# Optimization experiments

Hardware: AMD Instinct MI355X
Metric: run time of the kernel (lower is better)

Reference implementation:

```python
import jax, jax.numpy as jnp
import numpy as np

N, C, W_DIM, H_DIM = 2, 256, 64, 64
HEADS = 4
DH = C // HEADS  # per-head dim for Q,K,V projections
EPS = 1e-5


def _layernorm(x, w, b):
    mu = jnp.mean(x, axis=-1, keepdims=True)
    var = jnp.var(x, axis=-1, keepdims=True)
    return (x - mu) * jax.lax.rsqrt(var + EPS) * w + b


def setup_inputs() -> dict:
    key = jax.random.key(0)
    ks = jax.random.split(key, 12)
    s = 1.0 / np.sqrt(C)
    return {
        "x": jax.random.normal(ks[0], (N, C, W_DIM, H_DIM), dtype=jnp.float32),
        "ln1_w": jnp.ones((C,), jnp.float32),
        "ln1_b": jnp.zeros((C,), jnp.float32),
        # per-head projection weights, laid out for x @ W: [heads, C, DH]
        "WQ": jax.random.normal(ks[1], (HEADS, C, DH), jnp.float32) * s,
        "WK": jax.random.normal(ks[2], (HEADS, C, DH), jnp.float32) * s,
        "WV": jax.random.normal(ks[3], (HEADS, C, DH), jnp.float32) * s,
        "ln2_w": jnp.ones((C,), jnp.float32),
        "ln2_b": jnp.zeros((C,), jnp.float32),
        "W1": jax.random.normal(ks[4], (C, C), jnp.float32) * s,
        "b1": jnp.zeros((C,), jnp.float32),
        "W2": jax.random.normal(ks[5], (C, C), jnp.float32) * s,
        "b2": jnp.zeros((C,), jnp.float32),
    }


def reference(x, ln1_w, ln1_b, WQ, WK, WV, ln2_w, ln2_b, W1, b1, W2, b2):
    n, c, w, h = x.shape
    s = w * h
    # 'n c w h -> n (w h) c'
    r = x.reshape(n, c, s).transpose(0, 2, 1)          # [n, s, c]
    norm = _layernorm(r, ln1_w, ln1_b)
    # all heads at once (original loops over heads)
    Q = jnp.einsum('nsc,hcd->nhsd', norm, WQ)
    K = jnp.einsum('nsc,hcd->nhsd', norm, WK)
    V = jnp.einsum('nsc,hcd->nhsd', norm, WV)
    # scale is 1/sqrt(seq_len) per original (keys.shape[1])
    y = jnp.einsum('nhqd,nhkd->nhqk', Q, K) / jnp.sqrt(jnp.float32(s))
    # QUIRK: softmax over dim=1 of [n, q, k] => the QUERY axis (axis=2 here)
    z = jax.nn.softmax(y, axis=2)
    attn = jnp.einsum('nhqk,nhkd->nhqd', z, V)         # [n, h, s, dh]
    attn_cat = attn.transpose(0, 2, 1, 3).reshape(n, s, c)
    out = attn_cat + r
    out = _layernorm(out, ln2_w, ln2_b)
    out = jax.nn.gelu(out @ W1 + b1, approximate=False) @ W2 + b2
    out = out + attn_cat
    # 'n (w h) c -> n c w h'
    return out.transpose(0, 2, 1).reshape(n, c, w, h)
```

## Files before the change

kernel.cpp:

```cpp
#include <hip/hip_runtime.h>
#include <math.h>

#define SEQ 4096
#define CH  256
#define NHT 8
#define DHD 64

#define QSCALE 0.0225421092f

using bf16x8 = __attribute__((ext_vector_type(8))) short;
using f32x4  = __attribute__((ext_vector_type(4))) float;
typedef unsigned short u16;
typedef unsigned int   u32;

__device__ __forceinline__ u16 f2bf(float f) {
    u32 u = __float_as_uint(f);
    u = (u + 0x7fffu + ((u >> 16) & 1u)) >> 16;
    return (u16)u;
}
__device__ __forceinline__ float bf2f(u16 h) {
    return __uint_as_float(((u32)h) << 16);
}
__device__ __forceinline__ float fexp2(float x) {
    return __builtin_amdgcn_exp2f(x);
}

__global__ __launch_bounds__(256) void k_prep(const float* __restrict__ x,
                                              const float* __restrict__ ln1w,
                                              const float* __restrict__ ln1b,
                                              const float* __restrict__ WQ,
                                              const float* __restrict__ WK,
                                              const float* __restrict__ WV,
                                              const float* __restrict__ W1,
                                              const float* __restrict__ W2,
                                              u16* __restrict__ norm,
                                              u16* __restrict__ BtQKV,
                                              u16* __restrict__ W1t,
                                              u16* __restrict__ W2t)
{
    __shared__ float tile[32][257];
    __shared__ float mu[32], rs[32];
    int bid = blockIdx.x;
    int t = threadIdx.x;
    if (bid < 1280) {
        int id = bid * 256 + t;
        if (id < 768 * 256) {
            int j = id >> 8, c = id & 255;
            int which = j >> 8, h = (j >> 6) & 3, d = j & 63;
            const float* W = (which == 0) ? WQ : (which == 1) ? WK : WV;
            BtQKV[id] = f2bf(W[(h * 256 + c) * 64 + d]);
        } else if (id < 768 * 256 + 65536) {
            int jj = id - 768 * 256;
            int j = jj >> 8, c = jj & 255;
            W1t[jj] = f2bf(W1[c * 256 + j]);
        } else if (id < 768 * 256 + 2 * 65536) {
            int jj = id - 768 * 256 - 65536;
            int j = jj >> 8, c = jj & 255;
            W2t[jj] = f2bf(W2[c * 256 + j]);
        }
        return;
    }
    int b2i = bid - 1280;
    int n = b2i >> 7, s0 = (b2i & 127) * 32;
    int sl = t & 31, cg = t >> 5;
    for (int cc = 0; cc < 256; cc += 8) {
        int c = cc + cg;
        tile[sl][c] = x[(n * 256 + c) * SEQ + s0 + sl];
    }
    __syncthreads();
    int wv = t >> 6, l = t & 63;
    for (int rr = 0; rr < 8; rr++) {
        int s = wv * 8 + rr;
        float a0 = tile[s][l], a1 = tile[s][l + 64], a2 = tile[s][l + 128], a3 = tile[s][l + 192];
        float sm = a0 + a1 + a2 + a3;
        float sq = a0 * a0 + a1 * a1 + a2 * a2 + a3 * a3;
        for (int off = 32; off; off >>= 1) { sm += __shfl_xor(sm, off); sq += __shfl_xor(sq, off); }
        if (l == 0) {
            float m = sm * (1.f / 256.f);
            mu[s] = m;
            rs[s] = rsqrtf(sq * (1.f / 256.f) - m * m + 1e-5f);
        }
    }
    __syncthreads();
    float ww = ln1w[t], bb = ln1b[t];
    for (int s = 0; s < 32; s++) {
        float v = (tile[s][t] - mu[s]) * rs[s] * ww + bb;
        norm[(n * SEQ + s0 + s) * 256 + t] = f2bf(v);
    }
}

__global__ __launch_bounds__(256) void k_qkv(const u16* __restrict__ norm,
                                             const u16* __restrict__ Bt,
                                             u16* __restrict__ Qo,
                                             u16* __restrict__ Ko,
                                             u16* __restrict__ Vto)
{
    int m0 = blockIdx.x * 64, j0 = blockIdx.y * 128;
    int t = threadIdx.x, w = t >> 6, lane = t & 63, quad = lane >> 4, l16 = lane & 15;
    const u16* Ap = norm + (long)(m0 + w * 16 + l16) * 256;
    const u16* Bp = Bt + (long)j0 * 256;
    f32x4 z = {0.f, 0.f, 0.f, 0.f};
    f32x4 acc[8];
    #pragma unroll
    for (int j = 0; j < 8; j++) acc[j] = z;
    #pragma unroll
    for (int kc = 0; kc < 8; kc++) {
        bf16x8 a = *(const bf16x8*)&Ap[kc * 32 + quad * 8];
        #pragma unroll
        for (int j = 0; j < 8; j++) {
            bf16x8 b = *(const bf16x8*)&Bp[(long)(j * 16 + l16) * 256 + kc * 32 + quad * 8];
            acc[j] = __builtin_amdgcn_mfma_f32_16x16x32_bf16(a, b, acc[j], 0, 0, 0);
        }
    }
    #pragma unroll
    for (int j = 0; j < 8; j++) {
        int col = j0 + j * 16 + l16;
        int which = col >> 8, h = (col >> 6) & 3, d = col & 63;
        int m = m0 + w * 16 + quad * 4;
        int n = m >> 12, s = m & 4095;
        if (which == 2) {
            u16 h0 = f2bf(acc[j][0]), h1 = f2bf(acc[j][1]);
            u16 h2_ = f2bf(acc[j][2]), h3 = f2bf(acc[j][3]);
            uint2 pk;
            pk.x = (u32)h0 | ((u32)h1 << 16);
            pk.y = (u32)h2_ | ((u32)h3 << 16);
            *(uint2*)&Vto[((long)(n * 4 + h) * 64 + d) * SEQ + s] = pk;
        } else {
            u16* dst = (which == 0) ? Qo : Ko;
            float sc = (which == 0) ? QSCALE : 1.0f;
            #pragma unroll
            for (int r = 0; r < 4; r++)
                dst[((n * 4 + h) * SEQ + s + r) * 64 + d] = f2bf(acc[j][r] * sc);
        }
    }
}

__global__ __launch_bounds__(256) void k_pass1(const u16* __restrict__ Q,
                                               const u16* __restrict__ Km,
                                               float* __restrict__ D2)
{
    __shared__ float Dred[128];
    int nh = blockIdx.y, k0 = blockIdx.x * 128, qc = blockIdx.z;
    const u16* Qh = Q + (long)nh * SEQ * 64;
    const u16* Kh = Km + (long)nh * SEQ * 64;
    int t = threadIdx.x, w = t >> 6, lane = t & 63, quad = lane >> 4, l16 = lane & 15;
    bf16x8 Kf[8][2];
    #pragma unroll
    for (int i = 0; i < 8; i++) {
        Kf[i][0] = *(const bf16x8*)&Kh[(k0 + i * 16 + l16) * 64 + quad * 8];
        Kf[i][1] = *(const bf16x8*)&Kh[(k0 + i * 16 + l16) * 64 + 32 + quad * 8];
    }
    if (t < 128) Dred[t] = 0.f;
    f32x4 z = {0.f, 0.f, 0.f, 0.f};
    float Dacc[8][4] = {};
    const int qw0 = qc * 2048 + w * 512;
    bf16x8 b0 = *(const bf16x8*)&Qh[(qw0 + l16) * 64 + quad * 8];
    bf16x8 b1 = *(const bf16x8*)&Qh[(qw0 + l16) * 64 + 32 + quad * 8];
    for (int step = 0; step < 32; step++) {
        int q = qw0 + step * 16;
        bf16x8 n0, n1;
        if (step < 31) {
            n0 = *(const bf16x8*)&Qh[(q + 16 + l16) * 64 + quad * 8];
            n1 = *(const bf16x8*)&Qh[(q + 16 + l16) * 64 + 32 + quad * 8];
        }
        #pragma unroll
        for (int i = 0; i < 8; i++) {
            f32x4 acc = z;
            acc = __builtin_amdgcn_mfma_f32_16x16x32_bf16(Kf[i][0], b0, acc, 0, 0, 0);
            acc = __builtin_amdgcn_mfma_f32_16x16x32_bf16(Kf[i][1], b1, acc, 0, 0, 0);
            #pragma unroll
            for (int r = 0; r < 4; r++) Dacc[i][r] += fexp2(acc[r]);
        }
        b0 = n0; b1 = n1;
    }
    #pragma unroll
    for (int i = 0; i < 8; i++)
        #pragma unroll
        for (int r = 0; r < 4; r++) {
            float v = Dacc[i][r];
            v += __shfl_xor(v, 1); v += __shfl_xor(v, 2);
            v += __shfl_xor(v, 4); v += __shfl_xor(v, 8);
            Dacc[i][r] = v;
        }
    __syncthreads();
    if (l16 == 0) {
        #pragma unroll
        for (int i = 0; i < 8; i++)
            #pragma unroll
            for (int r = 0; r < 4; r++)
                atomicAdd(&Dred[i * 16 + quad * 4 + r], Dacc[i][r]);
    }
    __syncthreads();
    if (t < 128) D2[((long)(qc * NHT + nh)) * SEQ + k0 + t] = Dred[t];
}

__global__ __launch_bounds__(256, 1) void k_pass2(const u16* __restrict__ Q,
                                                  const u16* __restrict__ Km,
                                                  const u16* __restrict__ Vt,
                                                  const float* __restrict__ D2,
                                                  float* __restrict__ acat2)
{
    __shared__ __align__(16) u16 lPA[4][128][36];
    __shared__ __align__(16) u16 lPB[4][128][36];
    __shared__ float Lk[2048];
    float (*red)[68] = (float(*)[68])lPA;

    int nh = blockIdx.y, q0 = blockIdx.x * 128, kcid = blockIdx.z;
    int n = nh >> 2, h = nh & 3;
    const u16* Qh = Q + (long)nh * SEQ * 64;
    const u16* Kh = Km + (long)nh * SEQ * 64;
    const u16* Vh = Vt + (long)nh * 64 * SEQ;
    int t = threadIdx.x, w = t >> 6, lane = t & 63, quad = lane >> 4, l16 = lane & 15;
    const int kw0 = kcid * 2048 + w * 512;
    const int klw = w * 512;

    {
        const float* Dp = D2 + (long)nh * SEQ + kcid * 2048;
        const long QS = (long)NHT * SEQ;
        #pragma unroll
        for (int off = 0; off < 8; off++) {
            int kl = off * 256 + t;
            Lk[kl] = __log2f(Dp[kl] + Dp[QS + kl]);
        }
    }
    bf16x8 Qf[8][2];
    #pragma unroll
    for (int jq = 0; jq < 8; jq++)
        #pragma unroll
        for (int ch = 0; ch < 2; ch++)
            Qf[jq][ch] = *(const bf16x8*)&Qh[(q0 + jq * 16 + l16) * 64 + ch * 32 + quad * 8];
    bf16x8 kA[2][2];
    #pragma unroll
    for (int ksub = 0; ksub < 2; ksub++) {
        kA[ksub][0] = *(const bf16x8*)&Kh[(kw0 + ksub * 16 + l16) * 64 + quad * 8];
        kA[ksub][1] = *(const bf16x8*)&Kh[(kw0 + ksub * 16 + l16) * 64 + 32 + quad * 8];
    }
    bf16x8 vb[4];
    #pragma unroll
    for (int jd = 0; jd < 4; jd++)
        vb[jd] = *(const bf16x8*)&Vh[(jd * 16 + l16) * SEQ + kw0 + quad * 8];
    f32x4 z = {0.f, 0.f, 0.f, 0.f};
    f32x4 accO[8][4];
    #pragma unroll
    for (int jq = 0; jq < 8; jq++)
        #pragma unroll
        for (int jd = 0; jd < 4; jd++) accO[jq][jd] = z;
    __syncthreads();

#define QK_PHASE(I, LPD)                                                      \
    {                                                                         \
        const int _i = (I);                                                   \
        _Pragma("unroll")                                                     \
        for (int ksub = 0; ksub < 2; ksub++) {                                \
            f32x4 Lv = *(const f32x4*)&Lk[klw + _i * 32 + ksub * 16 + quad * 4]; \
            _Pragma("unroll")                                                 \
            for (int jq = 0; jq < 8; jq++) {                                  \
                f32x4 acc = z;                                                \
                acc = __builtin_amdgcn_mfma_f32_16x16x32_bf16(kA[ksub][0], Qf[jq][0], acc, 0, 0, 0); \
                acc = __builtin_amdgcn_mfma_f32_16x16x32_bf16(kA[ksub][1], Qf[jq][1], acc, 0, 0, 0); \
                u32 e0 = __float_as_uint(fexp2(acc[0] - Lv[0]));              \
                u32 e1 = __float_as_uint(fexp2(acc[1] - Lv[1]));              \
                u32 e2 = __float_as_uint(fexp2(acc[2] - Lv[2]));              \
                u32 e3 = __float_as_uint(fexp2(acc[3] - Lv[3]));              \
                uint2 pk;                                                     \
                pk.x = __builtin_amdgcn_perm(e1, e0, 0x07060302u);            \
                pk.y = __builtin_amdgcn_perm(e3, e2, 0x07060302u);            \
                *(uint2*)&LPD[w][jq * 16 + l16][ksub * 16 + quad * 4] = pk;   \
            }                                                                 \
        }                                                                     \
        if (_i < 15) {                                                        \
            int kn = kw0 + _i * 32 + 32;                                      \
            _Pragma("unroll")                                                 \
            for (int ksub = 0; ksub < 2; ksub++) {                            \
                kA[ksub][0] = *(const bf16x8*)&Kh[(kn + ksub * 16 + l16) * 64 + quad * 8]; \
                kA[ksub][1] = *(const bf16x8*)&Kh[(kn + ksub * 16 + l16) * 64 + 32 + quad * 8]; \
            }                                                                 \
        }                                                                     \
    }

#define PV_PHASE(I, LPS)                                                      \
    {                                                                         \
        const int _i = (I);                                                   \
        _Pragma("unroll")                                                     \
        for (int jq = 0; jq < 8; jq++) {                                      \
            bf16x8 pa = *(const bf16x8*)&LPS[w][jq * 16 + l16][quad * 8];     \
            _Pragma("unroll")                                                 \
            for (int jd = 0; jd < 4; jd++)                                    \
                accO[jq][jd] = __builtin_amdgcn_mfma_f32_16x16x32_bf16(pa, vb[jd], accO[jq][jd], 0, 0, 0); \
        }                                                                     \
        if (_i < 15) {                                                        \
            int kn = kw0 + _i * 32 + 32;                                      \
            _Pragma("unroll")                                                 \
            for (int jd = 0; jd < 4; jd++)                                    \
                vb[jd] = *(const bf16x8*)&Vh[(jd * 16 + l16) * SEQ + kn + quad * 8]; \
        }                                                                     \
    }

    QK_PHASE(0, lPA)
    for (int tt = 0; tt < 7; tt++) {
        int i = tt * 2;
        QK_PHASE(i + 1, lPB)
        PV_PHASE(i,     lPA)
        QK_PHASE(i + 2, lPA)
        PV_PHASE(i + 1, lPB)
    }
    QK_PHASE(15, lPB)
    PV_PHASE(14, lPA)
    PV_PHASE(15, lPB)

#undef QK_PHASE
#undef PV_PHASE

    __syncthreads();
    for (int src = 0; src < 4; src++) {
        if (w == src) {
            #pragma unroll
            for (int jq = 0; jq < 8; jq++)
                #pragma unroll
                for (int jd = 0; jd < 4; jd++)
                    #pragma unroll
                    for (int r = 0; r < 4; r++) {
                        float* cell = &red[jq * 16 + quad * 4 + r][jd * 16 + l16];
                        if (src == 0) *cell = accO[jq][jd][r];
                        else          *cell += accO[jq][jd][r];
                    }
        }
        __syncthreads();
    }
    float* dst = acat2 + (long)kcid * 8192 * 256;
    #pragma unroll
    for (int p = 0; p < 8; p++) {
        int row = p * 16 + (t >> 4);
        int ch = (t & 15) * 4;
        float4 o = *(float4*)&red[row][ch];
        *(float4*)&dst[((long)n * SEQ + q0 + row) * 256 + h * 64 + ch] = o;
    }
}

__global__ __launch_bounds__(256) void k_tail(const float* __restrict__ x,
                                              const float* __restrict__ acat2,
                                              const float* __restrict__ lnw,
                                              const float* __restrict__ lnb,
                                              const u16* __restrict__ W1t,
                                              const float* __restrict__ b1v,
                                              const u16* __restrict__ W2t,
                                              const float* __restrict__ b2v,
                                              float* __restrict__ out)
{
    __shared__ __align__(16) unsigned char smem[16448];
    float (*tile)[257] = (float(*)[257])smem;
    u16 (*lT)[264] = (u16(*)[264])smem;
    __shared__ float aF[16][257];
    __shared__ float mu[16], rs[16];
    __shared__ __align__(16) u16 lH[16][264];

    const long STRIDE = (long)8192 * 256;
    int m0 = blockIdx.x * 16;
    int n = m0 >> 12, s0 = m0 & 4095;
    int t = threadIdx.x, w = t >> 6, lane = t & 63, quad = lane >> 4, l16 = lane & 15;

    {
        int sl = t & 15, cg = t >> 4;
        for (int cc = 0; cc < 256; cc += 16) {
            int c = cc + cg;
            tile[sl][c] = x[(n * 256 + c) * SEQ + s0 + sl];
        }
    }
    __syncthreads();
    for (int s = 0; s < 16; s++) {
        long idx = (long)(m0 + s) * 256 + t;
        float a = acat2[idx] + acat2[idx + STRIDE];
        aF[s][t] = a;
        tile[s][t] += a;
    }
    __syncthreads();
    {
        int l = t & 63;
        for (int rr = 0; rr < 4; rr++) {
            int s = w * 4 + rr;
            float a0 = tile[s][l], a1 = tile[s][l + 64], a2 = tile[s][l + 128], a3 = tile[s][l + 192];
            float sm = a0 + a1 + a2 + a3;
            float sq = a0 * a0 + a1 * a1 + a2 * a2 + a3 * a3;
            for (int off = 32; off; off >>= 1) { sm += __shfl_xor(sm, off); sq += __shfl_xor(sq, off); }
            if (l == 0) {
                float m = sm * (1.f / 256.f);
                mu[s] = m;
                rs[s] = rsqrtf(sq * (1.f / 256.f) - m * m + 1e-5f);
            }
        }
    }
    __syncthreads();
    {
        float ww = lnw[t], bb = lnb[t];
        for (int s = 0; s < 16; s++)
            lH[s][t] = f2bf((tile[s][t] - mu[s]) * rs[s] * ww + bb);
    }
    __syncthreads();

    f32x4 z = {0.f, 0.f, 0.f, 0.f};
    f32x4 acc1[4];
    #pragma unroll
    for (int js = 0; js < 4; js++) acc1[js] = z;
    #pragma unroll
    for (int kc = 0; kc < 8; kc++) {
        bf16x8 b = *(const bf16x8*)&lH[l16][kc * 32 + quad * 8];
        #pragma unroll
        for (int js = 0; js < 4; js++) {
            bf16x8 a = *(const bf16x8*)&W1t[(long)(w * 64 + js * 16 + l16) * 256 + kc * 32 + quad * 8];
            acc1[js] = __builtin_amdgcn_mfma_f32_16x16x32_bf16(a, b, acc1[js], 0, 0, 0);
        }
    }
    #pragma unroll
    for (int js = 0; js < 4; js++) {
        u32 e[4];
        #pragma unroll
        for (int r = 0; r < 4; r++) {
            int j = w * 64 + js * 16 + quad * 4 + r;
            float v = acc1[js][r] + b1v[j];
            float g = 0.5f * v * (1.f + erff(v * 0.70710678118f));
            u32 u = __float_as_uint(g);
            e[r] = u + 0x7fffu + ((u >> 16) & 1u);
        }
        uint2 pk;
        pk.x = __builtin_amdgcn_perm(e[1], e[0], 0x07060302u);
        pk.y = __builtin_amdgcn_perm(e[3], e[2], 0x07060302u);
        *(uint2*)&lT[l16][w * 64 + js * 16 + quad * 4] = pk;
    }
    __syncthreads();
    f32x4 acc2[4];
    #pragma unroll
    for (int cs = 0; cs < 4; cs++) acc2[cs] = z;
    #pragma unroll
    for (int kc = 0; kc < 8; kc++) {
        bf16x8 pa = *(const bf16x8*)&lT[l16][kc * 32 + quad * 8];
        #pragma unroll
        for (int cs = 0; cs < 4; cs++) {
            bf16x8 wb = *(const bf16x8*)&W2t[(long)(w * 64 + cs * 16 + l16) * 256 + kc * 32 + quad * 8];
            acc2[cs] = __builtin_amdgcn_mfma_f32_16x16x32_bf16(pa, wb, acc2[cs], 0, 0, 0);
        }
    }
    #pragma unroll
    for (int cs = 0; cs < 4; cs++) {
        int c = w * 64 + cs * 16 + l16;
        float bj = b2v[c];
        float vv[4];
        #pragma unroll
        for (int r = 0; r < 4; r++)
            vv[r] = acc2[cs][r] + bj + aF[quad * 4 + r][c];
        float4 o = make_float4(vv[0], vv[1], vv[2], vv[3]);
        *(float4*)&out[((long)n * 256 + c) * SEQ + s0 + quad * 4] = o;
    }
}

extern "C" void kernel_launch(void* const* d_in, const int* in_sizes, int n_in,
                              void* d_out, int out_size, void* d_ws, size_t ws_size,
                              hipStream_t stream) {
    const float* x    = (const float*)d_in[0];
    const float* ln1w = (const float*)d_in[1];
    const float* ln1b = (const float*)d_in[2];
    const float* WQ   = (const float*)d_in[3];
    const float* WK   = (const float*)d_in[4];
    const float* WV   = (const float*)d_in[5];
    const float* ln2w = (const float*)d_in[6];
    const float* ln2b = (const float*)d_in[7];
    const float* W1   = (const float*)d_in[8];
    const float* b1   = (const float*)d_in[9];
    const float* W2   = (const float*)d_in[10];
    const float* b2   = (const float*)d_in[11];
    float* out = (float*)d_out;

    char* p = (char*)d_ws;
    u16* norm   = (u16*)p;   p += (size_t)8192 * 256 * 2;
    u16* BtQKV  = (u16*)p;   p += (size_t)768 * 256 * 2;
    u16* W1t    = (u16*)p;   p += (size_t)256 * 256 * 2;
    u16* W2t    = (u16*)p;   p += (size_t)256 * 256 * 2;
    u16* Qb     = (u16*)p;   p += (size_t)NHT * SEQ * 64 * 2;
    u16* Kb     = (u16*)p;   p += (size_t)NHT * SEQ * 64 * 2;
    u16* VtT    = (u16*)p;   p += (size_t)NHT * SEQ * 64 * 2;
    float* D2   = (float*)p; p += (size_t)2 * NHT * SEQ * 4;
    float* acat2= (float*)p; p += (size_t)2 * 8192 * 256 * 4;

    k_prep<<<1536, 256, 0, stream>>>(x, ln1w, ln1b, WQ, WK, WV, W1, W2,
                                     norm, BtQKV, W1t, W2t);
    k_qkv<<<dim3(128, 6), 256, 0, stream>>>(norm, BtQKV, Qb, Kb, VtT);
    k_pass1<<<dim3(32, 8, 2), 256, 0, stream>>>(Qb, Kb, D2);
    k_pass2<<<dim3(32, 8, 2), 256, 0, stream>>>(Qb, Kb, VtT, D2, acat2);
    k_tail<<<512, 256, 0, stream>>>(x, acat2, ln2w, ln2b, W1t, b1, W2t, b2, out);
}
```

Measured before the change: 237.1 us.

## Fold softmax denominator into V and remap attention grid per XCD

The per-key softmax normaliser is no longer subtracted as a log inside the pass2 inner loop. A new kernel divides V by the key-wise denominator and converts it to bf16, so pass2 becomes plain exp2 followed by PV. V is now written as fp32 into the acat2 scratch buffer, adding a kernel launch and extra memory traffic. Pass1 and pass2 also use a 1D grid decoded so each XCD gets contiguous heads for L2 locality, and their software pipelining is restructured with one LDS buffer and double-buffered register K/V. Removing the LDS double buffer adds a possible hazard in reuse of the lP tile.

Measured after the change: 236.8 us. No clear change (-0.1%).

```diff
diff --git a/kernel.cpp b/kernel.cpp
--- a/kernel.cpp
+++ b/kernel.cpp
@@ -93,7 +93,7 @@
                                              const u16* __restrict__ Bt,
                                              u16* __restrict__ Qo,
                                              u16* __restrict__ Ko,
-                                             u16* __restrict__ Vto)
+                                             float* __restrict__ Vfo)
 {
     int m0 = blockIdx.x * 64, j0 = blockIdx.y * 128;
     int t = threadIdx.x, w = t >> 6, lane = t & 63, quad = lane >> 4, l16 = lane & 15;
@@ -119,12 +119,8 @@
         int m = m0 + w * 16 + quad * 4;
         int n = m >> 12, s = m & 4095;
         if (which == 2) {
-            u16 h0 = f2bf(acc[j][0]), h1 = f2bf(acc[j][1]);
-            u16 h2_ = f2bf(acc[j][2]), h3 = f2bf(acc[j][3]);
-            uint2 pk;
-            pk.x = (u32)h0 | ((u32)h1 << 16);
-            pk.y = (u32)h2_ | ((u32)h3 << 16);
-            *(uint2*)&Vto[((long)(n * 4 + h) * 64 + d) * SEQ + s] = pk;
+            float4 o = make_float4(acc[j][0], acc[j][1], acc[j][2], acc[j][3]);
+            *(float4*)&Vfo[((long)(n * 4 + h) * 64 + d) * SEQ + s] = o;
         } else {
             u16* dst = (which == 0) ? Qo : Ko;
             float sc = (which == 0) ? QSCALE : 1.0f;
@@ -135,12 +131,20 @@
     }
 }
 
+__device__ __forceinline__ void xcd_decode(int s, int& g, int& sub) {
+    int xcd = s & 7, m = s >> 3;
+    g = xcd * 2 + (m >> 5);
+    sub = m & 31;
+}
+
 __global__ __launch_bounds__(256) void k_pass1(const u16* __restrict__ Q,
                                                const u16* __restrict__ Km,
                                                float* __restrict__ D2)
 {
     __shared__ float Dred[128];
-    int nh = blockIdx.y, k0 = blockIdx.x * 128, qc = blockIdx.z;
+    int g, sub;
+    xcd_decode(blockIdx.x, g, sub);
+    int nh = g & 7, qc = g >> 3, k0 = sub * 128;
     const u16* Qh = Q + (long)nh * SEQ * 64;
     const u16* Kh = Km + (long)nh * SEQ * 64;
     int t = threadIdx.x, w = t >> 6, lane = t & 63, quad = lane >> 4, l16 = lane & 15;
@@ -154,25 +158,37 @@
     f32x4 z = {0.f, 0.f, 0.f, 0.f};
     float Dacc[8][4] = {};
     const int qw0 = qc * 2048 + w * 512;
-    bf16x8 b0 = *(const bf16x8*)&Qh[(qw0 + l16) * 64 + quad * 8];
-    bf16x8 b1 = *(const bf16x8*)&Qh[(qw0 + l16) * 64 + 32 + quad * 8];
-    for (int step = 0; step < 32; step++) {
-        int q = qw0 + step * 16;
-        bf16x8 n0, n1;
-        if (step < 31) {
-            n0 = *(const bf16x8*)&Qh[(q + 16 + l16) * 64 + quad * 8];
-            n1 = *(const bf16x8*)&Qh[(q + 16 + l16) * 64 + 32 + quad * 8];
-        }
-        #pragma unroll
-        for (int i = 0; i < 8; i++) {
-            f32x4 acc = z;
-            acc = __builtin_amdgcn_mfma_f32_16x16x32_bf16(Kf[i][0], b0, acc, 0, 0, 0);
-            acc = __builtin_amdgcn_mfma_f32_16x16x32_bf16(Kf[i][1], b1, acc, 0, 0, 0);
-            #pragma unroll
-            for (int r = 0; r < 4; r++) Dacc[i][r] += fexp2(acc[r]);
-        }
-        b0 = n0; b1 = n1;
-    }
+
+#define P1_LOADQ(B0, B1, ST)                                                  \
+    {                                                                         \
+        int _q = qw0 + (ST) * 16 + l16;                                       \
+        B0 = *(const bf16x8*)&Qh[_q * 64 + quad * 8];                         \
+        B1 = *(const bf16x8*)&Qh[_q * 64 + 32 + quad * 8];                    \
+    }
+#define P1_STEP(B0, B1)                                                       \
+    {                                                                         \
+        _Pragma("unroll")                                                     \
+        for (int i = 0; i < 8; i++) {                                         \
+            f32x4 acc = z;                                                    \
+            acc = __builtin_amdgcn_mfma_f32_16x16x32_bf16(Kf[i][0], B0, acc, 0, 0, 0); \
+            acc = __builtin_amdgcn_mfma_f32_16x16x32_bf16(Kf[i][1], B1, acc, 0, 0, 0); \
+            _Pragma("unroll")                                                 \
+            for (int r = 0; r < 4; r++) Dacc[i][r] += fexp2(acc[r]);          \
+        }                                                                     \
+    }
+
+    bf16x8 qa0, qa1, qb0, qb1;
+    P1_LOADQ(qa0, qa1, 0)
+    P1_LOADQ(qb0, qb1, 1)
+    for (int st = 0; st < 32; st += 2) {
+        P1_STEP(qa0, qa1)
+        if (st + 2 < 32) { P1_LOADQ(qa0, qa1, st + 2) }
+        P1_STEP(qb0, qb1)
+        if (st + 3 < 32) { P1_LOADQ(qb0, qb1, st + 3) }
+    }
+#undef P1_LOADQ
+#undef P1_STEP
+
     #pragma unroll
     for (int i = 0; i < 8; i++)
         #pragma unroll
@@ -194,122 +210,136 @@
     if (t < 128) D2[((long)(qc * NHT + nh)) * SEQ + k0 + t] = Dred[t];
 }
 
+__global__ __launch_bounds__(256) void k_vdiv(const float* __restrict__ Vf,
+                                              const float* __restrict__ D2,
+                                              u16* __restrict__ Vto)
+{
+    int b = blockIdx.x;
+    int nh = b >> 6, d = b & 63;
+    const float* Da = D2 + (long)nh * SEQ;
+    const float* Db = Da + (long)NHT * SEQ;
+    const float* src = Vf + ((long)nh * 64 + d) * SEQ;
+    u16* dst = Vto + ((long)nh * 64 + d) * SEQ;
+    int t = threadIdx.x;
+    #pragma unroll
+    for (int half = 0; half < 2; half++) {
+        int k = half * 2048 + t * 8;
+        float4 va = *(const float4*)&src[k];
+        float4 vb = *(const float4*)&src[k + 4];
+        float4 a0 = *(const float4*)&Da[k], a1 = *(const float4*)&Da[k + 4];
+        float4 b0 = *(const float4*)&Db[k], b1 = *(const float4*)&Db[k + 4];
+        float o[8];
+        o[0] = va.x / (a0.x + b0.x); o[1] = va.y / (a0.y + b0.y);
+        o[2] = va.z / (a0.z + b0.z); o[3] = va.w / (a0.w + b0.w);
+        o[4] = vb.x / (a1.x + b1.x); o[5] = vb.y / (a1.y + b1.y);
+        o[6] = vb.z / (a1.z + b1.z); o[7] = vb.w / (a1.w + b1.w);
+        uint4 pk;
+        pk.x = (u32)f2bf(o[0]) | ((u32)f2bf(o[1]) << 16);
+        pk.y = (u32)f2bf(o[2]) | ((u32)f2bf(o[3]) << 16);
+        pk.z = (u32)f2bf(o[4]) | ((u32)f2bf(o[5]) << 16);
+        pk.w = (u32)f2bf(o[6]) | ((u32)f2bf(o[7]) << 16);
+        *(uint4*)&dst[k] = pk;
+    }
+}
+
 __global__ __launch_bounds__(256, 1) void k_pass2(const u16* __restrict__ Q,
                                                   const u16* __restrict__ Km,
                                                   const u16* __restrict__ Vt,
-                                                  const float* __restrict__ D2,
                                                   float* __restrict__ acat2)
 {
-    __shared__ __align__(16) u16 lPA[4][128][36];
-    __shared__ __align__(16) u16 lPB[4][128][36];
-    __shared__ float Lk[2048];
-    float (*red)[68] = (float(*)[68])lPA;
-
-    int nh = blockIdx.y, q0 = blockIdx.x * 128, kcid = blockIdx.z;
+    __shared__ __align__(16) u16 lP[4][128][36];
+    float (*red)[68] = (float(*)[68])lP;
+
+    int g, sub;
+    xcd_decode(blockIdx.x, g, sub);
+    int nh = g & 7, kcid = g >> 3, q0 = sub * 128;
     int n = nh >> 2, h = nh & 3;
     const u16* Qh = Q + (long)nh * SEQ * 64;
     const u16* Kh = Km + (long)nh * SEQ * 64;
     const u16* Vh = Vt + (long)nh * 64 * SEQ;
     int t = threadIdx.x, w = t >> 6, lane = t & 63, quad = lane >> 4, l16 = lane & 15;
     const int kw0 = kcid * 2048 + w * 512;
-    const int klw = w * 512;
-
-    {
-        const float* Dp = D2 + (long)nh * SEQ + kcid * 2048;
-        const long QS = (long)NHT * SEQ;
-        #pragma unroll
-        for (int off = 0; off < 8; off++) {
-            int kl = off * 256 + t;
-            Lk[kl] = __log2f(Dp[kl] + Dp[QS + kl]);
-        }
-    }
+
     bf16x8 Qf[8][2];
     #pragma unroll
     for (int jq = 0; jq < 8; jq++)
         #pragma unroll
         for (int ch = 0; ch < 2; ch++)
             Qf[jq][ch] = *(const bf16x8*)&Qh[(q0 + jq * 16 + l16) * 64 + ch * 32 + quad * 8];
-    bf16x8 kA[2][2];
-    #pragma unroll
-    for (int ksub = 0; ksub < 2; ksub++) {
-        kA[ksub][0] = *(const bf16x8*)&Kh[(kw0 + ksub * 16 + l16) * 64 + quad * 8];
-        kA[ksub][1] = *(const bf16x8*)&Kh[(kw0 + ksub * 16 + l16) * 64 + 32 + quad * 8];
-    }
-    bf16x8 vb[4];
-    #pragma unroll
-    for (int jd = 0; jd < 4; jd++)
-        vb[jd] = *(const bf16x8*)&Vh[(jd * 16 + l16) * SEQ + kw0 + quad * 8];
+
     f32x4 z = {0.f, 0.f, 0.f, 0.f};
     f32x4 accO[8][4];
     #pragma unroll
     for (int jq = 0; jq < 8; jq++)
         #pragma unroll
         for (int jd = 0; jd < 4; jd++) accO[jq][jd] = z;
-    __syncthreads();
-
-#define QK_PHASE(I, LPD)                                                      \
+
+#define LOAD_K(KA, KPOS)                                                      \
     {                                                                         \
-        const int _i = (I);                                                   \
         _Pragma("unroll")                                                     \
         for (int ksub = 0; ksub < 2; ksub++) {                                \
-            f32x4 Lv = *(const f32x4*)&Lk[klw + _i * 32 + ksub * 16 + quad * 4]; \
+            KA[ksub][0] = *(const bf16x8*)&Kh[((KPOS) + ksub * 16 + l16) * 64 + quad * 8];      \
+            KA[ksub][1] = *(const bf16x8*)&Kh[((KPOS) + ksub * 16 + l16) * 64 + 32 + quad * 8]; \
+        }                                                                     \
+    }
+#define LOAD_V(VB, KPOS)                                                      \
+    {                                                                         \
+        _Pragma("unroll")                                                     \
+        for (int jd = 0; jd < 4; jd++)                                        \
+            VB[jd] = *(const bf16x8*)&Vh[(jd * 16 + l16) * SEQ + (KPOS) + quad * 8]; \
+    }
+#define QK_SLAB(KA)                                                           \
+    {                                                                         \
+        _Pragma("unroll")                                                     \
+        for (int ksub = 0; ksub < 2; ksub++) {                                \
             _Pragma("unroll")                                                 \
             for (int jq = 0; jq < 8; jq++) {                                  \
                 f32x4 acc = z;                                                \
-                acc = __builtin_amdgcn_mfma_f32_16x16x32_bf16(kA[ksub][0], Qf[jq][0], acc, 0, 0, 0); \
-                acc = __builtin_amdgcn_mfma_f32_16x16x32_bf16(kA[ksub][1], Qf[jq][1], acc, 0, 0, 0); \
-                u32 e0 = __float_as_uint(fexp2(acc[0] - Lv[0]));              \
-                u32 e1 = __float_as_uint(fexp2(acc[1] - Lv[1]));              \
-                u32 e2 = __float_as_uint(fexp2(acc[2] - Lv[2]));              \
-                u32 e3 = __float_as_uint(fexp2(acc[3] - Lv[3]));              \
+                acc = __builtin_amdgcn_mfma_f32_16x16x32_bf16(KA[ksub][0], Qf[jq][0], acc, 0, 0, 0); \
+                acc = __builtin_amdgcn_mfma_f32_16x16x32_bf16(KA[ksub][1], Qf[jq][1], acc, 0, 0, 0); \
+                u32 e0 = __float_as_uint(fexp2(acc[0]));                      \
+                u32 e1 = __float_as_uint(fexp2(acc[1]));                      \
+                u32 e2 = __float_as_uint(fexp2(acc[2]));                      \
+                u32 e3 = __float_as_uint(fexp2(acc[3]));                      \
                 uint2 pk;                                                     \
                 pk.x = __builtin_amdgcn_perm(e1, e0, 0x07060302u);            \
                 pk.y = __builtin_amdgcn_perm(e3, e2, 0x07060302u);            \
-                *(uint2*)&LPD[w][jq * 16 + l16][ksub * 16 + quad * 4] = pk;   \
+                *(uint2*)&lP[w][jq * 16 + l16][ksub * 16 + quad * 4] = pk;    \
             }                                                                 \
         }                                                                     \
-        if (_i < 15) {                                                        \
-            int kn = kw0 + _i * 32 + 32;                                      \
-            _Pragma("unroll")                                                 \
-            for (int ksub = 0; ksub < 2; ksub++) {                            \
-                kA[ksub][0] = *(const bf16x8*)&Kh[(kn + ksub * 16 + l16) * 64 + quad * 8]; \
-                kA[ksub][1] = *(const bf16x8*)&Kh[(kn + ksub * 16 + l16) * 64 + 32 + quad * 8]; \
-            }                                                                 \
-        }                                                                     \
-    }
-
-#define PV_PHASE(I, LPS)                                                      \
+    }
+#define PV_SLAB(VB)                                                           \
     {                                                                         \
-        const int _i = (I);                                                   \
         _Pragma("unroll")                                                     \
         for (int jq = 0; jq < 8; jq++) {                                      \
-            bf16x8 pa = *(const bf16x8*)&LPS[w][jq * 16 + l16][quad * 8];     \
+            bf16x8 pa = *(const bf16x8*)&lP[w][jq * 16 + l16][quad * 8];      \
             _Pragma("unroll")                                                 \
             for (int jd = 0; jd < 4; jd++)                                    \
-                accO[jq][jd] = __builtin_amdgcn_mfma_f32_16x16x32_bf16(pa, vb[jd], accO[jq][jd], 0, 0, 0); \
+                accO[jq][jd] = __builtin_amdgcn_mfma_f32_16x16x32_bf16(pa, VB[jd], accO[jq][jd], 0, 0, 0); \
         }                                                                     \
-        if (_i < 15) {                                                        \
-            int kn = kw0 + _i * 32 + 32;                                      \
-            _Pragma("unroll")                                                 \
-            for (int jd = 0; jd < 4; jd++)                                    \
-                vb[jd] = *(const bf16x8*)&Vh[(jd * 16 + l16) * SEQ + kn + quad * 8]; \
-        }                                                                     \
-    }
-
-    QK_PHASE(0, lPA)
-    for (int tt = 0; tt < 7; tt++) {
-        int i = tt * 2;
-        QK_PHASE(i + 1, lPB)
-        PV_PHASE(i,     lPA)
-        QK_PHASE(i + 2, lPA)
-        PV_PHASE(i + 1, lPB)
-    }
-    QK_PHASE(15, lPB)
-    PV_PHASE(14, lPA)
-    PV_PHASE(15, lPB)
-
-#undef QK_PHASE
-#undef PV_PHASE
+    }
+
+    bf16x8 kA0[2][2], kA1[2][2], vb0[4], vb1[4];
+    LOAD_K(kA0, kw0)
+    LOAD_V(vb0, kw0)
+    LOAD_K(kA1, kw0 + 32)
+    LOAD_V(vb1, kw0 + 32)
+
+    for (int tt = 0; tt < 8; tt++) {
+        int kf = kw0 + tt * 64;
+        QK_SLAB(kA0)
+        if (tt < 7) { LOAD_K(kA0, kf + 64) }
+        PV_SLAB(vb0)
+        if (tt < 7) { LOAD_V(vb0, kf + 64) }
+        QK_SLAB(kA1)
+        if (tt < 7) { LOAD_K(kA1, kf + 96) }
+        PV_SLAB(vb1)
+        if (tt < 7) { LOAD_V(vb1, kf + 96) }
+    }
+#undef LOAD_K
+#undef LOAD_V
+#undef QK_SLAB
+#undef PV_SLAB
 
     __syncthreads();
     for (int src = 0; src < 4; src++) {
@@ -479,11 +509,13 @@
     u16* VtT    = (u16*)p;   p += (size_t)NHT * SEQ * 64 * 2;
     float* D2   = (float*)p; p += (size_t)2 * NHT * SEQ * 4;
     float* acat2= (float*)p; p += (size_t)2 * 8192 * 256 * 4;
+    float* Vf   = acat2;
 
     k_prep<<<1536, 256, 0, stream>>>(x, ln1w, ln1b, WQ, WK, WV, W1, W2,
                                      norm, BtQKV, W1t, W2t);
-    k_qkv<<<dim3(128, 6), 256, 0, stream>>>(norm, BtQKV, Qb, Kb, VtT);
-    k_pass1<<<dim3(32, 8, 2), 256, 0, stream>>>(Qb, Kb, D2);
-    k_pass2<<<dim3(32, 8, 2), 256, 0, stream>>>(Qb, Kb, VtT, D2, acat2);
+    k_qkv<<<dim3(128, 6), 256, 0, stream>>>(norm, BtQKV, Qb, Kb, Vf);
+    k_pass1<<<512, 256, 0, stream>>>(Qb, Kb, D2);
+    k_vdiv<<<512, 256, 0, stream>>>(Vf, D2, VtT);
+    k_pass2<<<512, 256, 0, stream>>>(Qb, Kb, VtT, acat2);
     k_tail<<<512, 256, 0, stream>>>(x, acat2, ln2w, ln2b, W1t, b1, W2t, b2, out);
 }
```
